# Kernel optimization log

Measured on AMD Instinct MI355X. Metric: run time of the kernel, lower is better.

## Reference

```python
import jax, jax.numpy as jnp
import numpy as np

B, S, D = 4, 2048, 1024

def setup_inputs() -> dict:
    key = jax.random.key(0)
    ks = jax.random.split(key, 7)
    s = 1.0 / np.sqrt(D)
    return {
        "x": jax.random.normal(ks[0], (B, S, D), dtype=jnp.float32),
        "Wk": jax.random.uniform(ks[1], (D, D), jnp.float32, -s, s),
        "bk": jax.random.uniform(ks[2], (D,), jnp.float32, -s, s),
        "Wq": jax.random.uniform(ks[3], (D, D), jnp.float32, -s, s),
        "bq": jax.random.uniform(ks[4], (D,), jnp.float32, -s, s),
        "Wv": jax.random.uniform(ks[5], (D, D), jnp.float32, -s, s),
        "bv": jax.random.uniform(ks[6], (D,), jnp.float32, -s, s),
    }

def reference(x, Wk, bk, Wq, bq, Wv, bv):
    # Linear projections (torch Linear: x @ W.T + b; here weights stored as [in, out])
    k = jnp.einsum('bsd,de->bse', x, Wk) + bk
    q = jnp.einsum('bsd,de->bse', x, Wq) + bq
    v = jnp.einsum('bsd,de->bse', x, Wv) + bv
    scale = jnp.asarray(q.shape[-1], q.dtype) ** 0.5
    scores = jnp.einsum('bqd,bkd->bqk', q, k) / scale  # [B,S,S]
    attn = jax.nn.softmax(scores, axis=-1)
    y = jnp.einsum('bqk,bkd->bqd', attn, v)
    return y
```

## Files before the change

kernel.cpp:

```cpp
#include <hip/hip_runtime.h>
#include <hip/hip_bf16.h>


typedef __attribute__((ext_vector_type(8))) short short8;
typedef __attribute__((ext_vector_type(4))) float f32x4;

__device__ __forceinline__ unsigned short f2b(float f) {
    unsigned u = __builtin_bit_cast(unsigned, f);
    unsigned r = 0x7FFFu + ((u >> 16) & 1u);
    return (unsigned short)((u + r) >> 16);
}
__device__ __forceinline__ float b2f(unsigned short h) {
    return __builtin_bit_cast(float, ((unsigned)h) << 16);
}

__device__ __forceinline__ void gload16(const void* g, void* lds_uniform_base) {
    __builtin_amdgcn_global_load_lds(
        (const __attribute__((address_space(1))) unsigned int*)(unsigned long long)g,
        (__attribute__((address_space(3))) unsigned int*)(unsigned)(unsigned long long)lds_uniform_base,
        16, 0, 0);
}

__global__ void cvt_x(const float* __restrict__ x, unsigned short* __restrict__ xb) {
    int i = blockIdx.x * 256 + threadIdx.x;
    float4 v = ((const float4*)x)[i];
    ushort4 o;
    o.x = f2b(v.x); o.y = f2b(v.y); o.z = f2b(v.z); o.w = f2b(v.w);
    ((ushort4*)xb)[i] = o;
}

__global__ void transpose_w(const float* __restrict__ w0, const float* __restrict__ w1,
                            const float* __restrict__ w2, unsigned short* __restrict__ wt) {
    const float* W = (blockIdx.z == 0) ? w0 : (blockIdx.z == 1) ? w1 : w2;
    __shared__ float t[32][33];
    int k0 = blockIdx.y * 32, n0 = blockIdx.x * 32;
    int tx = threadIdx.x, ty = threadIdx.y;
#pragma unroll
    for (int i = 0; i < 4; i++)
        t[ty * 4 + i][tx] = W[(size_t)(k0 + ty * 4 + i) * 1024 + n0 + tx];
    __syncthreads();
    unsigned short* out = wt + (size_t)blockIdx.z * 1024 * 1024;
#pragma unroll
    for (int i = 0; i < 4; i++)
        out[(size_t)(n0 + ty * 4 + i) * 1024 + k0 + tx] = f2b(t[tx][ty * 4 + i]);
}

template <int BN, int MODE>
__global__ __launch_bounds__(512, 2) void gemm2(
    const unsigned short* __restrict__ A, const unsigned short* __restrict__ Bm,
    void* __restrict__ Cv, const float* __restrict__ bias,
    int N, int K, long long sA, long long sB, long long sC, float alpha) {
    constexpr int FN = BN / 64;
    __shared__ unsigned short As[2][256 * 64];
    __shared__ unsigned short Bs[2][BN * 64];
    const int tid = threadIdx.x;
    const int wave = tid >> 6, lane = tid & 63;

    const int gx = gridDim.x, gy = gridDim.y;
    const int nwg = gx * gy * (int)gridDim.z;
    const int orig = blockIdx.x + gx * (blockIdx.y + gy * blockIdx.z);
    const int q8 = nwg >> 3, r8 = nwg & 7;
    const int xcd = orig & 7, sub = orig >> 3;
    const int wg = (xcd < r8 ? xcd * (q8 + 1) : r8 * (q8 + 1) + (xcd - r8) * q8) + sub;
    const int bx = wg % gx;
    const int tmp = wg / gx;
    const int by = tmp % gy, bz = tmp / gy;

    const int m0 = by * 256, n0 = bx * BN;
    A += (long long)bz * sA;
    Bm += (long long)bz * sB;

    const int wm = wave >> 2, wn = wave & 3;
    const int l16 = lane & 15;
    const int lk = (lane >> 4) << 3;

    f32x4 acc[8][FN];
#pragma unroll
    for (int m = 0; m < 8; m++)
#pragma unroll
        for (int n = 0; n < FN; n++) acc[m][n] = (f32x4){0.f, 0.f, 0.f, 0.f};

    auto STAGE = [&](int buf, int t) {
        const int k0 = t << 6;
#pragma unroll
        for (int j = 0; j < 4; j++) {
            int cid = tid + j * 512;
            int row = cid >> 3, kk = (cid & 7) << 3;
            gload16(A + (size_t)(m0 + row) * K + k0 + kk,
                    (char*)&As[buf][0] + wave * 1024 + j * 8192);
        }
#pragma unroll
        for (int j = 0; j < FN; j++) {
            int cid = tid + j * 512;
            int row = cid >> 3, kk = (cid & 7) << 3;
            gload16(Bm + (size_t)(n0 + row) * K + k0 + kk,
                    (char*)&Bs[buf][0] + wave * 1024 + j * 8192);
        }
    };

    const int nt = K >> 6;
    int cur = 0;
    STAGE(0, 0);
    __syncthreads();
    for (int t = 0; t < nt; ++t) {
        if (t + 1 < nt) STAGE(cur ^ 1, t + 1);
#pragma unroll
        for (int ks = 0; ks < 2; ks++) {
            short8 af[8], bf[FN];
#pragma unroll
            for (int m = 0; m < 8; m++)
                af[m] = *(const short8*)&As[cur][(wm * 128 + m * 16 + l16) * 64 + ks * 32 + lk];
#pragma unroll
            for (int n = 0; n < FN; n++)
                bf[n] = *(const short8*)&Bs[cur][(wn * (BN / 4) + n * 16 + l16) * 64 + ks * 32 + lk];
#pragma unroll
            for (int m = 0; m < 8; m++)
#pragma unroll
                for (int n = 0; n < FN; n++)
                    acc[m][n] = __builtin_amdgcn_mfma_f32_16x16x32_bf16(af[m], bf[n], acc[m][n], 0, 0, 0);
        }
        __syncthreads();
        cur ^= 1;
    }

    const int rowb0 = m0 + wm * 128 + ((lane >> 4) << 2);
    const int colb0 = n0 + wn * (BN / 4) + l16;
#pragma unroll
    for (int m = 0; m < 8; m++) {
#pragma unroll
        for (int n = 0; n < FN; n++) {
            int col = colb0 + n * 16;
            int rowb = rowb0 + m * 16;
            float bv_ = bias ? bias[col] : 0.f;
            if (MODE == 0) {
                unsigned short* C = (unsigned short*)Cv + (long long)bz * sC;
#pragma unroll
                for (int i = 0; i < 4; i++)
                    C[(size_t)(rowb + i) * N + col] = f2b(acc[m][n][i] * alpha + bv_);
            } else if (MODE == 2) {
                float* C = (float*)Cv + (long long)bz * sC;
#pragma unroll
                for (int i = 0; i < 4; i++)
                    C[(size_t)(rowb + i) * N + col] = acc[m][n][i] * alpha + bv_;
            } else {
                int b = rowb >> 11, s = rowb & 2047;
                ushort4 pk;
                pk.x = f2b(acc[m][n][0] * alpha + bv_);
                pk.y = f2b(acc[m][n][1] * alpha + bv_);
                pk.z = f2b(acc[m][n][2] * alpha + bv_);
                pk.w = f2b(acc[m][n][3] * alpha + bv_);
                *(ushort4*)((unsigned short*)Cv + (size_t)b * (1024 * 2048) + (size_t)col * 2048 + s) = pk;
            }
        }
    }
}

__global__ __launch_bounds__(256) void softmax_inplace(unsigned short* __restrict__ sc) {
    const size_t row = blockIdx.x;
    unsigned short* p = sc + row * 2048;
    const int tid = threadIdx.x;
    const int wave = tid >> 6, lane = tid & 63;
    short8 raw = *(const short8*)&p[tid * 8];
    float f[8];
#pragma unroll
    for (int i = 0; i < 8; i++) f[i] = b2f((unsigned short)raw[i]);
    float mx = f[0];
#pragma unroll
    for (int i = 1; i < 8; i++) mx = fmaxf(mx, f[i]);
#pragma unroll
    for (int o = 32; o > 0; o >>= 1) mx = fmaxf(mx, __shfl_xor(mx, o, 64));
    __shared__ float red[8];
    if (lane == 0) red[wave] = mx;
    __syncthreads();
    mx = fmaxf(fmaxf(red[0], red[1]), fmaxf(red[2], red[3]));
    float e[8], s = 0.f;
#pragma unroll
    for (int i = 0; i < 8; i++) { e[i] = __expf(f[i] - mx); s += e[i]; }
#pragma unroll
    for (int o = 32; o > 0; o >>= 1) s += __shfl_xor(s, o, 64);
    if (lane == 0) red[4 + wave] = s;
    __syncthreads();
    s = (red[4] + red[5]) + (red[6] + red[7]);
    float r = 1.0f / s;
    short8 outv;
#pragma unroll
    for (int i = 0; i < 8; i++) outv[i] = (short)f2b(e[i] * r);
    *(short8*)&p[tid * 8] = outv;
}

extern "C" void kernel_launch(void* const* d_in, const int* in_sizes, int n_in,
                              void* d_out, int out_size, void* d_ws, size_t ws_size,
                              hipStream_t stream) {
    const float* x  = (const float*)d_in[0];
    const float* Wk = (const float*)d_in[1];
    const float* bk = (const float*)d_in[2];
    const float* Wq = (const float*)d_in[3];
    const float* bq = (const float*)d_in[4];
    const float* Wv = (const float*)d_in[5];
    const float* bv = (const float*)d_in[6];
    float* out = (float*)d_out;

    char* ws = (char*)d_ws;
    unsigned short* xb  = (unsigned short*)(ws);
    unsigned short* wt  = (unsigned short*)(ws + 16777216);
    unsigned short* kb  = (unsigned short*)(ws + 23068672);
    unsigned short* qb  = (unsigned short*)(ws + 39845888);
    unsigned short* vtb = (unsigned short*)(ws + 56623104);
    unsigned short* sc  = (unsigned short*)(ws + 73400320);

    cvt_x<<<8192, 256, 0, stream>>>(x, xb);
    transpose_w<<<dim3(32, 32, 3), dim3(32, 8), 0, stream>>>(Wk, Wq, Wv, wt);

    gemm2<128, 0><<<dim3(8, 32, 1), 512, 0, stream>>>(xb, wt + 0 * 1048576, kb, bk,
                                                      1024, 1024, 0, 0, 0, 1.f);
    gemm2<128, 0><<<dim3(8, 32, 1), 512, 0, stream>>>(xb, wt + 1 * 1048576, qb, bq,
                                                      1024, 1024, 0, 0, 0, 1.f);
    gemm2<128, 1><<<dim3(8, 32, 1), 512, 0, stream>>>(xb, wt + 2 * 1048576, vtb, bv,
                                                      1024, 1024, 0, 0, 0, 1.f);

    gemm2<256, 0><<<dim3(8, 8, 4), 512, 0, stream>>>(qb, kb, sc, nullptr,
                                                     2048, 1024,
                                                     2048LL * 1024, 2048LL * 1024, 2048LL * 2048,
                                                     0.03125f);
    softmax_inplace<<<8192, 256, 0, stream>>>(sc);

    gemm2<128, 2><<<dim3(8, 8, 4), 512, 0, stream>>>(sc, vtb, out, nullptr,
                                                     1024, 2048,
                                                     2048LL * 2048, 1024LL * 2048, 2048LL * 1024,
                                                     1.f);
}
```

Measured before the change: 294.6 us.

## Rewrite GEMM as 256x256 eight-phase pipelined kernel and fuse QKV projections

Replaces the double-buffered GEMM with a 256x256 tile kernel. It splits each K tile into quarter-chunk global-to-LDS loads interleaved with MFMA phases, using explicit barriers, vmcnt/lgkmcnt waits and setprio. The three Q/K/V projections become one launch over a concatenated N=3072 weight, with each column routed to its own output and layout. The aim is better overlap of memory and compute and fewer launches. The cost is fewer workgroups for the PV GEMM (128 blocks) and more fragile hand-placed synchronization.

Result: slower. 326.2 us (+10.7%).

```diff
diff --git a/kernel.cpp b/kernel.cpp
--- a/kernel.cpp
+++ b/kernel.cpp
@@ -20,6 +20,10 @@
         (__attribute__((address_space(3))) unsigned int*)(unsigned)(unsigned long long)lds_uniform_base,
         16, 0, 0);
 }
+
+#define BARRIER __builtin_amdgcn_s_barrier()
+#define WAIT_LGKM0 do { asm volatile("s_waitcnt lgkmcnt(0)" ::: "memory"); __builtin_amdgcn_sched_barrier(0); } while (0)
+#define WAIT_VM(n) do { asm volatile("s_waitcnt vmcnt(" #n ")" ::: "memory"); __builtin_amdgcn_sched_barrier(0); } while (0)
 
 __global__ void cvt_x(const float* __restrict__ x, unsigned short* __restrict__ xb) {
     int i = blockIdx.x * 256 + threadIdx.x;
@@ -45,14 +49,15 @@
         out[(size_t)(n0 + ty * 4 + i) * 1024 + k0 + tx] = f2b(t[tx][ty * 4 + i]);
 }
 
-template <int BN, int MODE>
-__global__ __launch_bounds__(512, 2) void gemm2(
+template <int MODE>
+__global__ __launch_bounds__(512, 2) void gemm8(
     const unsigned short* __restrict__ A, const unsigned short* __restrict__ Bm,
-    void* __restrict__ Cv, const float* __restrict__ bias,
+    void* __restrict__ C0, void* __restrict__ C1, void* __restrict__ C2,
+    const float* __restrict__ bias0, const float* __restrict__ bias1,
+    const float* __restrict__ bias2,
     int N, int K, long long sA, long long sB, long long sC, float alpha) {
-    constexpr int FN = BN / 64;
     __shared__ unsigned short As[2][256 * 64];
-    __shared__ unsigned short Bs[2][BN * 64];
+    __shared__ unsigned short Bs[2][256 * 64];
     const int tid = threadIdx.x;
     const int wave = tid >> 6, lane = tid & 63;
 
@@ -66,90 +71,154 @@
     const int tmp = wg / gx;
     const int by = tmp % gy, bz = tmp / gy;
 
-    const int m0 = by * 256, n0 = bx * BN;
+    const int m0 = by * 256, n0 = bx * 256;
     A += (long long)bz * sA;
     Bm += (long long)bz * sB;
 
     const int wm = wave >> 2, wn = wave & 3;
     const int l16 = lane & 15;
     const int lk = (lane >> 4) << 3;
-
-    f32x4 acc[8][FN];
+    const int nt = K >> 6;
+
+    f32x4 acc[8][4];
 #pragma unroll
     for (int m = 0; m < 8; m++)
 #pragma unroll
-        for (int n = 0; n < FN; n++) acc[m][n] = (f32x4){0.f, 0.f, 0.f, 0.f};
-
-    auto STAGE = [&](int buf, int t) {
-        const int k0 = t << 6;
-#pragma unroll
-        for (int j = 0; j < 4; j++) {
-            int cid = tid + j * 512;
-            int row = cid >> 3, kk = (cid & 7) << 3;
-            gload16(A + (size_t)(m0 + row) * K + k0 + kk,
-                    (char*)&As[buf][0] + wave * 1024 + j * 8192);
-        }
-#pragma unroll
-        for (int j = 0; j < FN; j++) {
-            int cid = tid + j * 512;
-            int row = cid >> 3, kk = (cid & 7) << 3;
-            gload16(Bm + (size_t)(n0 + row) * K + k0 + kk,
-                    (char*)&Bs[buf][0] + wave * 1024 + j * 8192);
-        }
-    };
-
-    const int nt = K >> 6;
-    int cur = 0;
-    STAGE(0, 0);
-    __syncthreads();
-    for (int t = 0; t < nt; ++t) {
-        if (t + 1 < nt) STAGE(cur ^ 1, t + 1);
-#pragma unroll
-        for (int ks = 0; ks < 2; ks++) {
-            short8 af[8], bf[FN];
-#pragma unroll
-            for (int m = 0; m < 8; m++)
-                af[m] = *(const short8*)&As[cur][(wm * 128 + m * 16 + l16) * 64 + ks * 32 + lk];
-#pragma unroll
-            for (int n = 0; n < FN; n++)
-                bf[n] = *(const short8*)&Bs[cur][(wn * (BN / 4) + n * 16 + l16) * 64 + ks * 32 + lk];
-#pragma unroll
-            for (int m = 0; m < 8; m++)
-#pragma unroll
-                for (int n = 0; n < FN; n++)
-                    acc[m][n] = __builtin_amdgcn_mfma_f32_16x16x32_bf16(af[m], bf[n], acc[m][n], 0, 0, 0);
-        }
-        __syncthreads();
-        cur ^= 1;
+        for (int n = 0; n < 4; n++) acc[m][n] = (f32x4){0.f, 0.f, 0.f, 0.f};
+
+    const int strow = tid >> 3;
+    const int stkk = (tid & 7) << 3;
+
+    auto ST_A = [&](int bb, int c, int tt) {
+        if (tt >= nt) return;
+        gload16(A + (size_t)(m0 + c * 64 + strow) * K + (tt << 6) + stkk,
+                (char*)&As[bb][0] + c * 8192 + wave * 1024);
+    };
+    auto ST_B = [&](int bb, int c, int tt) {
+        if (tt >= nt) return;
+        gload16(Bm + (size_t)(n0 + c * 64 + strow) * K + (tt << 6) + stkk,
+                (char*)&Bs[bb][0] + c * 8192 + wave * 1024);
+    };
+
+    short8 af[4][2], bf0[2][2], bf1[2][2];
+    auto DS_A = [&](int bb, int mh) {
+#pragma unroll
+        for (int fm = 0; fm < 4; fm++)
+#pragma unroll
+            for (int ks = 0; ks < 2; ks++)
+                af[fm][ks] = *(const short8*)
+                    &As[bb][(wm * 128 + mh * 64 + fm * 16 + l16) * 64 + ks * 32 + lk];
+    };
+    auto DS_B = [&](int bb, int nh, short8 (&bf)[2][2]) {
+#pragma unroll
+        for (int fn = 0; fn < 2; fn++)
+#pragma unroll
+            for (int ks = 0; ks < 2; ks++)
+                bf[fn][ks] = *(const short8*)
+                    &Bs[bb][(wn * 64 + nh * 32 + fn * 16 + l16) * 64 + ks * 32 + lk];
+    };
+    auto MFMA16 = [&](int mh, int nh, short8 (&bf)[2][2]) {
+        __builtin_amdgcn_s_setprio(1);
+#pragma unroll
+        for (int fm = 0; fm < 4; fm++)
+#pragma unroll
+            for (int fn = 0; fn < 2; fn++)
+#pragma unroll
+                for (int ks = 0; ks < 2; ks++)
+                    acc[mh * 4 + fm][nh * 2 + fn] = __builtin_amdgcn_mfma_f32_16x16x32_bf16(
+                        af[fm][ks], bf[fn][ks], acc[mh * 4 + fm][nh * 2 + fn], 0, 0, 0);
+        __builtin_amdgcn_s_setprio(0);
+    };
+
+    ST_A(0, 0, 0); ST_A(0, 1, 0); ST_A(0, 2, 0); ST_A(0, 3, 0);
+    ST_B(0, 0, 0); ST_B(0, 1, 0); ST_B(0, 2, 0); ST_B(0, 3, 0);
+    ST_A(1, 0, 1); ST_A(1, 1, 1); ST_A(1, 2, 1); ST_A(1, 3, 1);
+    ST_B(1, 0, 1); ST_B(1, 1, 1);
+    WAIT_VM(6);
+    BARRIER;
+
+    for (int it = 0; it < (nt >> 1); ++it) {
+        const int t = it << 1;
+        const bool last = (t + 2 >= nt);
+        DS_A(0, 0); DS_B(0, 0, bf0);
+        ST_B(1, 2, t + 1); ST_B(1, 3, t + 1);
+        BARRIER; WAIT_LGKM0;
+        MFMA16(0, 0, bf0);
+        BARRIER;
+        DS_B(0, 1, bf1);
+        ST_A(0, 0, t + 2); ST_A(0, 2, t + 2);
+        BARRIER; WAIT_LGKM0;
+        MFMA16(0, 1, bf1);
+        BARRIER;
+        DS_A(0, 1);
+        ST_B(0, 0, t + 2); ST_B(0, 1, t + 2);
+        BARRIER; WAIT_LGKM0;
+        MFMA16(1, 0, bf0);
+        BARRIER;
+        ST_A(0, 1, t + 2); ST_A(0, 3, t + 2);
+        BARRIER;
+        MFMA16(1, 1, bf1);
+        if (last) { WAIT_VM(0); } else { WAIT_VM(6); }
+        BARRIER;
+        DS_A(1, 0); DS_B(1, 0, bf0);
+        ST_B(0, 2, t + 2); ST_B(0, 3, t + 2);
+        BARRIER; WAIT_LGKM0;
+        MFMA16(0, 0, bf0);
+        BARRIER;
+        DS_B(1, 1, bf1);
+        ST_A(1, 0, t + 3); ST_A(1, 2, t + 3);
+        BARRIER; WAIT_LGKM0;
+        MFMA16(0, 1, bf1);
+        BARRIER;
+        DS_A(1, 1);
+        ST_B(1, 0, t + 3); ST_B(1, 1, t + 3);
+        BARRIER; WAIT_LGKM0;
+        MFMA16(1, 0, bf0);
+        BARRIER;
+        ST_A(1, 1, t + 3); ST_A(1, 3, t + 3);
+        BARRIER;
+        MFMA16(1, 1, bf1);
+        if (last) { WAIT_VM(0); } else { WAIT_VM(6); }
+        BARRIER;
     }
 
     const int rowb0 = m0 + wm * 128 + ((lane >> 4) << 2);
-    const int colb0 = n0 + wn * (BN / 4) + l16;
 #pragma unroll
     for (int m = 0; m < 8; m++) {
 #pragma unroll
-        for (int n = 0; n < FN; n++) {
-            int col = colb0 + n * 16;
-            int rowb = rowb0 + m * 16;
-            float bv_ = bias ? bias[col] : 0.f;
+        for (int n = 0; n < 4; n++) {
+            const int row = rowb0 + m * 16;
+            const int col = n0 + wn * 64 + n * 16 + l16;
             if (MODE == 0) {
-                unsigned short* C = (unsigned short*)Cv + (long long)bz * sC;
+                unsigned short* C = (unsigned short*)C0 + (long long)bz * sC;
+                float bb = bias0 ? bias0[col] : 0.f;
 #pragma unroll
                 for (int i = 0; i < 4; i++)
-                    C[(size_t)(rowb + i) * N + col] = f2b(acc[m][n][i] * alpha + bv_);
+                    C[(size_t)(row + i) * N + col] = f2b(acc[m][n][i] * alpha + bb);
             } else if (MODE == 2) {
-                float* C = (float*)Cv + (long long)bz * sC;
+                float* C = (float*)C0 + (long long)bz * sC;
+                float bb = bias0 ? bias0[col] : 0.f;
 #pragma unroll
                 for (int i = 0; i < 4; i++)
-                    C[(size_t)(rowb + i) * N + col] = acc[m][n][i] * alpha + bv_;
+                    C[(size_t)(row + i) * N + col] = acc[m][n][i] * alpha + bb;
             } else {
-                int b = rowb >> 11, s = rowb & 2047;
-                ushort4 pk;
-                pk.x = f2b(acc[m][n][0] * alpha + bv_);
-                pk.y = f2b(acc[m][n][1] * alpha + bv_);
-                pk.z = f2b(acc[m][n][2] * alpha + bv_);
-                pk.w = f2b(acc[m][n][3] * alpha + bv_);
-                *(ushort4*)((unsigned short*)Cv + (size_t)b * (1024 * 2048) + (size_t)col * 2048 + s) = pk;
+                const int sel = col >> 10, lc = col & 1023;
+                const float bb = (sel == 0 ? bias0 : sel == 1 ? bias1 : bias2)[lc];
+                if (sel < 2) {
+                    unsigned short* C = (unsigned short*)(sel == 0 ? C0 : C1);
+#pragma unroll
+                    for (int i = 0; i < 4; i++)
+                        C[(size_t)(row + i) * 1024 + lc] = f2b(acc[m][n][i] + bb);
+                } else {
+                    const int b = row >> 11, s = row & 2047;
+                    ushort4 pk;
+                    pk.x = f2b(acc[m][n][0] + bb);
+                    pk.y = f2b(acc[m][n][1] + bb);
+                    pk.z = f2b(acc[m][n][2] + bb);
+                    pk.w = f2b(acc[m][n][3] + bb);
+                    *(ushort4*)((unsigned short*)C2 + (size_t)b * 2097152 +
+                                (size_t)lc * 2048 + s) = pk;
+                }
             }
         }
     }
@@ -211,21 +280,16 @@
     cvt_x<<<8192, 256, 0, stream>>>(x, xb);
     transpose_w<<<dim3(32, 32, 3), dim3(32, 8), 0, stream>>>(Wk, Wq, Wv, wt);
 
-    gemm2<128, 0><<<dim3(8, 32, 1), 512, 0, stream>>>(xb, wt + 0 * 1048576, kb, bk,
-                                                      1024, 1024, 0, 0, 0, 1.f);
-    gemm2<128, 0><<<dim3(8, 32, 1), 512, 0, stream>>>(xb, wt + 1 * 1048576, qb, bq,
-                                                      1024, 1024, 0, 0, 0, 1.f);
-    gemm2<128, 1><<<dim3(8, 32, 1), 512, 0, stream>>>(xb, wt + 2 * 1048576, vtb, bv,
-                                                      1024, 1024, 0, 0, 0, 1.f);
-
-    gemm2<256, 0><<<dim3(8, 8, 4), 512, 0, stream>>>(qb, kb, sc, nullptr,
-                                                     2048, 1024,
-                                                     2048LL * 1024, 2048LL * 1024, 2048LL * 2048,
-                                                     0.03125f);
+    gemm8<3><<<dim3(12, 32, 1), 512, 0, stream>>>(
+        xb, wt, kb, qb, vtb, bk, bq, bv, 3072, 1024, 0, 0, 0, 1.f);
+
+    gemm8<0><<<dim3(8, 8, 4), 512, 0, stream>>>(
+        qb, kb, sc, nullptr, nullptr, nullptr, nullptr, nullptr,
+        2048, 1024, 2048LL * 1024, 2048LL * 1024, 2048LL * 2048, 0.03125f);
+
     softmax_inplace<<<8192, 256, 0, stream>>>(sc);
 
-    gemm2<128, 2><<<dim3(8, 8, 4), 512, 0, stream>>>(sc, vtb, out, nullptr,
-                                                     1024, 2048,
-                                                     2048LL * 2048, 1024LL * 2048, 2048LL * 1024,
-                                                     1.f);
-}
+    gemm8<2><<<dim3(4, 8, 4), 512, 0, stream>>>(
+        sc, vtb, out, nullptr, nullptr, nullptr, nullptr, nullptr,
+        1024, 2048, 2048LL * 2048, 1024LL * 2048, 2048LL * 1024, 1.f);
+}
```
